# Kernel optimization log

Hardware: AMD Instinct MI355X
Metric: run time of the kernel (lower is better)

Reference implementation:

```python
import jax, jax.numpy as jnp
import numpy as np

CARRY_DIM = 384
READ_DIM = 128
D_MODEL = CARRY_DIM + READ_DIM  # 512
VOCAB = 128
NUM_FF = 7
B, T = 128, 1024


def _pm1(key, shape):
    # random +/-1 floats, matching random_pm1 in the torch source
    return jnp.where(jax.random.bernoulli(key, 0.5, shape), 1.0, -1.0).astype(jnp.float32)


def setup_inputs() -> dict:
    key = jax.random.key(0)
    k0, k1, k2, k3, k4 = jax.random.split(key, 5)
    return {
        "tokens": jax.random.randint(k0, (B, T), 0, VOCAB, dtype=jnp.int32),
        "initial": _pm1(k1, (D_MODEL,)),
        "embed": _pm1(k2, (VOCAB, READ_DIM)),
        "ff": _pm1(k3, (NUM_FF, D_MODEL, D_MODEL)),
        "ff_thresh": jnp.zeros((NUM_FF, D_MODEL), jnp.float32),
        "head": _pm1(k4, (READ_DIM, VOCAB)),
    }


def reference(tokens, initial, embed, ff, ff_thresh, head):
    # tokens:[B,T] int32; all params are +/-1 floats (the unpacked view of the
    # bit-packed int32 buffers; popcount GEMM == +/-1 matmul in integer arithmetic).
    b = tokens.shape[0]
    emb = jnp.swapaxes(embed[tokens], 0, 1)          # [T,B,READ_DIM]
    state0 = jnp.broadcast_to(initial, (b, D_MODEL))  # [B,512] +/-1

    def step(state, e):
        # replace read slice with current token embedding
        x = jnp.concatenate([state[:, :CARRY_DIM], e], axis=1)  # [B,512]

        def layer(xc, wt):
            w, t = wt  # w:[512,512], t:[512]
            # binary matmul (popcount dot in +/-1 space) + threshold nonlinearity
            return jnp.where(xc @ w >= t, 1.0, -1.0).astype(jnp.float32), None

        x, _ = jax.lax.scan(layer, x, (ff, ff_thresh))
        logits = x[:, CARRY_DIM:] @ head  # [B,VOCAB] integer-valued counts
        return x, logits

    _, logits = jax.lax.scan(step, state0, emb)  # logits:[T,B,V]
    return jnp.swapaxes(logits, 0, 1)            # [B,T,V]
```

## Files before the change

### kernel.cpp

```cpp
#include <hip/hip_runtime.h>
#include <hip/hip_bf16.h>
#include <stdint.h>
#include <math.h>

#define NUM_FF 7
#define DM 512
#define RD 128
#define VOCABN 128
#define BATCH 128
#define TLEN 1024

typedef unsigned int u32x4 __attribute__((ext_vector_type(4)));

__global__ void pack_ff_kernel(const float* __restrict__ ff, uint32_t* __restrict__ ffq) {
    int idx = blockIdx.x * blockDim.x + threadIdx.x;
    if (idx >= NUM_FF * 16 * DM) return;
    int j = idx & (DM - 1);
    int m = (idx >> 9) & 15;
    int l = idx >> 13;
    const float* base = ff + (size_t)l * DM * DM + (size_t)(m * 32) * DM + j;
    uint32_t w = 0;
#pragma unroll
    for (int i = 0; i < 32; ++i)
        w |= (base[(size_t)i * DM] > 0.0f ? 1u : 0u) << i;
    ffq[(l * 4 + (m >> 2)) * DM * 4 + j * 4 + (m & 3)] = w;
}

__global__ void pack_thresh_kernel(const float* __restrict__ th, int* __restrict__ it) {
    int idx = blockIdx.x * blockDim.x + threadIdx.x;
    if (idx < NUM_FF * DM)
        it[idx] = (int)floor((512.0 - (double)th[idx]) * 0.5);
}

__global__ void pack_small_kernel(const float* __restrict__ embed,
                                  const float* __restrict__ head,
                                  const float* __restrict__ initial,
                                  uint32_t* __restrict__ embp,
                                  uint32_t* __restrict__ headp,
                                  uint32_t* __restrict__ initp) {
    int idx = threadIdx.x;
    {
        int v = idx >> 2, k = idx & 3;
        uint32_t w = 0;
#pragma unroll
        for (int i = 0; i < 32; ++i)
            w |= (embed[v * RD + k * 32 + i] > 0.0f ? 1u : 0u) << i;
        embp[idx] = w;
    }
    {
        int k = idx >> 7, v = idx & 127;
        uint32_t w = 0;
#pragma unroll
        for (int i = 0; i < 32; ++i)
            w |= (head[(k * 32 + i) * VOCABN + v] > 0.0f ? 1u : 0u) << i;
        headp[idx] = w;
    }
    if (idx < 16) {
        uint32_t w = 0;
#pragma unroll
        for (int i = 0; i < 32; ++i)
            w |= (initial[idx * 32 + i] > 0.0f ? 1u : 0u) << i;
        initp[idx] = w;
    }
}

__device__ __forceinline__ int bdot4(uint4 s0, uint4 s1, uint4 s2, uint4 s3,
                                     u32x4 w0, u32x4 w1, u32x4 w2, u32x4 w3) {
    int a = __popc(s0.x ^ w0[0]);
    a += __popc(s0.y ^ w0[1]);
    a += __popc(s0.z ^ w0[2]);
    a += __popc(s0.w ^ w0[3]);
    a += __popc(s1.x ^ w1[0]);
    a += __popc(s1.y ^ w1[1]);
    a += __popc(s1.z ^ w1[2]);
    a += __popc(s1.w ^ w1[3]);
    int c = __popc(s2.x ^ w2[0]);
    c += __popc(s2.y ^ w2[1]);
    c += __popc(s2.z ^ w2[2]);
    c += __popc(s2.w ^ w2[3]);
    c += __popc(s3.x ^ w3[0]);
    c += __popc(s3.y ^ w3[1]);
    c += __popc(s3.z ^ w3[2]);
    c += __popc(s3.w ^ w3[3]);
    return a + c;
}

#define SYNCB asm volatile("s_waitcnt lgkmcnt(0)\n\ts_barrier" ::: "memory")

__attribute__((amdgpu_flat_work_group_size(512, 512), amdgpu_waves_per_eu(2, 2)))
__global__ void brnn_kernel(const int* __restrict__ tokens,
                            const uint32_t* __restrict__ ffq,
                            const int* __restrict__ ithr,
                            const uint32_t* __restrict__ embp,
                            const uint32_t* __restrict__ headp,
                            const uint32_t* __restrict__ initp,
                            float* __restrict__ out) {
    const int b = blockIdx.x;
    const int tid = threadIdx.x;
    const int wv = tid >> 6;
    const int lane = tid & 63;

    __shared__ uint4 xq0[4], xq1[4];
    __shared__ uint4 hx4;
    __shared__ uint32_t emb_lds[DM];
    __shared__ int tok_lds[TLEN + 2];

    u32x4 W00, W01, W02, W03, W10, W11, W12, W13, W20, W21, W22, W23,
          W30, W31, W32, W33, W40, W41, W42, W43, W50, W51, W52, W53,
          W60, W61, W62, W63;
#define WLOAD(V, L, Q) asm volatile("global_load_dwordx4 %0, %1, off" \
        : "=v"(V) : "v"(ffq + ((L) * 4 + (Q)) * (DM * 4) + tid * 4))
    WLOAD(W00, 0, 0); WLOAD(W01, 0, 1); WLOAD(W02, 0, 2); WLOAD(W03, 0, 3);
    WLOAD(W10, 1, 0); WLOAD(W11, 1, 1); WLOAD(W12, 1, 2); WLOAD(W13, 1, 3);
    WLOAD(W20, 2, 0); WLOAD(W21, 2, 1); WLOAD(W22, 2, 2); WLOAD(W23, 2, 3);
    WLOAD(W30, 3, 0); WLOAD(W31, 3, 1); WLOAD(W32, 3, 2); WLOAD(W33, 3, 3);
    WLOAD(W40, 4, 0); WLOAD(W41, 4, 1); WLOAD(W42, 4, 2); WLOAD(W43, 4, 3);
    WLOAD(W50, 5, 0); WLOAD(W51, 5, 1); WLOAD(W52, 5, 2); WLOAD(W53, 5, 3);
    WLOAD(W60, 6, 0); WLOAD(W61, 6, 1); WLOAD(W62, 6, 2); WLOAD(W63, 6, 3);
#undef WLOAD
    asm volatile("s_waitcnt vmcnt(0)" ::: "memory");

    const int it0 = ithr[0 * DM + tid];
    const int it1 = ithr[1 * DM + tid];
    const int it2 = ithr[2 * DM + tid];
    const int it3 = ithr[3 * DM + tid];
    const int it4 = ithr[4 * DM + tid];
    const int it5 = ithr[5 * DM + tid];
    const int it6 = ithr[6 * DM + tid];

    const int hvv = (wv << 4) | (lane & 15);
    const uint32_t h0 = headp[0 * VOCABN + hvv];
    const uint32_t h1 = headp[1 * VOCABN + hvv];
    const uint32_t h2 = headp[2 * VOCABN + hvv];
    const uint32_t h3 = headp[3 * VOCABN + hvv];

    emb_lds[tid] = embp[tid];
    tok_lds[tid] = tokens[b * TLEN + tid];
    tok_lds[tid + 512] = tokens[b * TLEN + tid + 512];
    if (tid == 0) { tok_lds[TLEN] = 0; tok_lds[TLEN + 1] = 0; }
    if (tid < 16) ((uint32_t*)xq0)[tid] = initp[tid];
    __syncthreads();
    if (tid < 4) ((uint32_t*)xq0)[12 + tid] = emb_lds[tok_lds[0] * 4 + tid];
    __syncthreads();

    float* outb = out + (size_t)b * TLEN * VOCABN;

#define LAYER(L, SRCQ, DSTQ) do {                                              \
        const uint4* xb_ = (const uint4*)(SRCQ);                               \
        uint4 s0 = xb_[0], s1 = xb_[1], s2 = xb_[2], s3 = xb_[3];              \
        int acc = bdot4(s0, s1, s2, s3, W##L##0, W##L##1, W##L##2, W##L##3);   \
        unsigned long long m = __ballot(acc <= it##L);                         \
        if (lane == 0)                                                         \
            ((uint2*)(DSTQ))[wv] = make_uint2((uint32_t)m, (uint32_t)(m >> 32)); \
        SYNCB;                                                                 \
    } while (0)

#define LAYERF(SRCQ, DSTQ) do {                                                \
        const uint4* xb_ = (const uint4*)(SRCQ);                               \
        uint4 s0 = xb_[0], s1 = xb_[1], s2 = xb_[2], s3 = xb_[3];              \
        int acc = bdot4(s0, s1, s2, s3, W60, W61, W62, W63);                   \
        unsigned long long m = __ballot(acc <= it6);                           \
        if (lane == 0) {                                                       \
            uint2 v_ = make_uint2((uint32_t)m, (uint32_t)(m >> 32));           \
            if (wv < 6) ((uint2*)(DSTQ))[wv] = v_;                             \
            else ((uint2*)&hx4)[wv - 6] = v_;                                  \
        }                                                                      \
        if (wv == 7 && lane < 4) ((uint32_t*)(DSTQ))[12 + lane] = embw;        \
        SYNCB;                                                                 \
    } while (0)

#define STEP(AQ, BQ, T) do {                                                   \
                      \
        uint32_t embw = 0;                                                     \
        if (wv == 7) embw = emb_lds[tok_lds[(T) + 1] * 4 + (lane & 3)];        \
        LAYER(0, AQ, BQ);                                                      \
        LAYER(1, BQ, AQ);                                                      \
        LAYER(2, AQ, BQ);                                                      \
        LAYER(3, BQ, AQ);                                                      \
        LAYER(4, AQ, BQ);                                                      \
        LAYER(5, BQ, AQ);                                                      \
        LAYERF(AQ, BQ);                                                        \
        uint4 hv_ = hx4;                                                       \
        if (lane < 16) {                                                       \
            int hc = __popc(hv_.x ^ h0) + __popc(hv_.y ^ h1) +                 \
                     __popc(hv_.z ^ h2) + __popc(hv_.w ^ h3);                  \
            outb[(T) * VOCABN + hvv] = (float)(RD - 2 * hc);                   \
        }                                                                      \
    } while (0)

    for (int t = 0; t < TLEN; t += 2) {
        STEP(xq0, xq1, t);
        STEP(xq1, xq0, t + 1);
    }
#undef LAYER
#undef LAYERF
#undef STEP
}

extern "C" void kernel_launch(void* const* d_in, const int* in_sizes, int n_in,
                              void* d_out, int out_size, void* d_ws, size_t ws_size,
                              hipStream_t stream) {
    const int* tokens = (const int*)d_in[0];
    const float* initial = (const float*)d_in[1];
    const float* embed = (const float*)d_in[2];
    const float* ff = (const float*)d_in[3];
    const float* ff_thresh = (const float*)d_in[4];
    const float* head = (const float*)d_in[5];
    float* out = (float*)d_out;

    uint32_t* ffq = (uint32_t*)d_ws;
    uint32_t* embp = ffq + NUM_FF * 16 * DM;
    uint32_t* headp = embp + 512;
    uint32_t* initp = headp + 512;
    int* ithr = (int*)(initp + 16);

    pack_ff_kernel<<<(NUM_FF * 16 * DM + 255) / 256, 256, 0, stream>>>(ff, ffq);
    pack_thresh_kernel<<<(NUM_FF * DM + 255) / 256, 256, 0, stream>>>(ff_thresh, ithr);
    pack_small_kernel<<<1, 512, 0, stream>>>(embed, head, initial, embp, headp, initp);
    brnn_kernel<<<BATCH, 512, 0, stream>>>(tokens, ffq, ithr, embp, headp, initp, out);
}
```

Baseline: 1.946 ms.

## Split each neuron's dot product across four lanes with DPP reduction and AGPR weights

```diff
diff --git a/kernel.cpp b/kernel.cpp
--- a/kernel.cpp
+++ b/kernel.cpp
@@ -13,17 +13,20 @@
 typedef unsigned int u32x4 __attribute__((ext_vector_type(4)));
 
 __global__ void pack_ff_kernel(const float* __restrict__ ff, uint32_t* __restrict__ ffq) {
-    int idx = blockIdx.x * blockDim.x + threadIdx.x;
-    if (idx >= NUM_FF * 16 * DM) return;
-    int j = idx & (DM - 1);
-    int m = (idx >> 9) & 15;
-    int l = idx >> 13;
-    const float* base = ff + (size_t)l * DM * DM + (size_t)(m * 32) * DM + j;
+    int o = blockIdx.x * blockDim.x + threadIdx.x;
+    if (o >= NUM_FF * 16 * DM) return;
+    int k = o & 3;
+    int t = (o >> 2) & (DM - 1);
+    int lq = o >> 11;
+    int l = lq >> 2, j = lq & 3;
+    int col = (t & ~3) + j;
+    int wi = 4 * (t & 3) + k;
+    const float* base = ff + (size_t)l * DM * DM + (size_t)(wi * 32) * DM + col;
     uint32_t w = 0;
 #pragma unroll
     for (int i = 0; i < 32; ++i)
         w |= (base[(size_t)i * DM] > 0.0f ? 1u : 0u) << i;
-    ffq[(l * 4 + (m >> 2)) * DM * 4 + j * 4 + (m & 3)] = w;
+    ffq[o] = w;
 }
 
 __global__ void pack_thresh_kernel(const float* __restrict__ th, int* __restrict__ it) {
@@ -39,16 +42,14 @@
                                   uint32_t* __restrict__ headp,
                                   uint32_t* __restrict__ initp) {
     int idx = threadIdx.x;
-    {
-        int v = idx >> 2, k = idx & 3;
+    {   int v = idx >> 2, k = idx & 3;
         uint32_t w = 0;
 #pragma unroll
         for (int i = 0; i < 32; ++i)
             w |= (embed[v * RD + k * 32 + i] > 0.0f ? 1u : 0u) << i;
         embp[idx] = w;
     }
-    {
-        int k = idx >> 7, v = idx & 127;
+    {   int k = idx >> 7, v = idx & 127;
         uint32_t w = 0;
 #pragma unroll
         for (int i = 0; i < 32; ++i)
@@ -64,28 +65,17 @@
     }
 }
 
-__device__ __forceinline__ int bdot4(uint4 s0, uint4 s1, uint4 s2, uint4 s3,
-                                     u32x4 w0, u32x4 w1, u32x4 w2, u32x4 w3) {
-    int a = __popc(s0.x ^ w0[0]);
-    a += __popc(s0.y ^ w0[1]);
-    a += __popc(s0.z ^ w0[2]);
-    a += __popc(s0.w ^ w0[3]);
-    a += __popc(s1.x ^ w1[0]);
-    a += __popc(s1.y ^ w1[1]);
-    a += __popc(s1.z ^ w1[2]);
-    a += __popc(s1.w ^ w1[3]);
-    int c = __popc(s2.x ^ w2[0]);
-    c += __popc(s2.y ^ w2[1]);
-    c += __popc(s2.z ^ w2[2]);
-    c += __popc(s2.w ^ w2[3]);
-    c += __popc(s3.x ^ w3[0]);
-    c += __popc(s3.y ^ w3[1]);
-    c += __popc(s3.z ^ w3[2]);
-    c += __popc(s3.w ^ w3[3]);
-    return a + c;
+__device__ __forceinline__ int dppadd(int v) {
+    v += __builtin_amdgcn_update_dpp(0, v, 0xB1, 0xF, 0xF, true);
+    v += __builtin_amdgcn_update_dpp(0, v, 0x4E, 0xF, 0xF, true);
+    return v;
 }
 
 #define SYNCB asm volatile("s_waitcnt lgkmcnt(0)\n\ts_barrier" ::: "memory")
+
+#define AW(D, S) asm volatile("v_accvgpr_write_b32 %0, %1" : "=a"(D) : "v"(S))
+#define AR(S) __extension__({ uint32_t r_; \
+        asm volatile("v_accvgpr_read_b32 %0, %1" : "=v"(r_) : "a"(S)); r_; })
 
 __attribute__((amdgpu_flat_work_group_size(512, 512), amdgpu_waves_per_eu(2, 2)))
 __global__ void brnn_kernel(const int* __restrict__ tokens,
@@ -99,21 +89,41 @@
     const int tid = threadIdx.x;
     const int wv = tid >> 6;
     const int lane = tid & 63;
+    const int lq4 = lane & 3;
 
     __shared__ uint4 xq0[4], xq1[4];
     __shared__ uint4 hx4;
     __shared__ uint32_t emb_lds[DM];
     __shared__ int tok_lds[TLEN + 2];
 
-    u32x4 W00, W01, W02, W03, W10, W11, W12, W13, W20, W21, W22, W23,
-          W30, W31, W32, W33, W40, W41, W42, W43, W50, W51, W52, W53,
-          W60, W61, W62, W63;
+    uint32_t A0_00,A0_01,A0_02,A0_03,A0_10,A0_11,A0_12,A0_13,
+             A0_20,A0_21,A0_22,A0_23,A0_30,A0_31,A0_32,A0_33;
+    uint32_t A1_00,A1_01,A1_02,A1_03,A1_10,A1_11,A1_12,A1_13,
+             A1_20,A1_21,A1_22,A1_23,A1_30,A1_31,A1_32,A1_33;
+    uint32_t A2_00,A2_01,A2_02,A2_03,A2_10,A2_11,A2_12,A2_13,
+             A2_20,A2_21,A2_22,A2_23,A2_30,A2_31,A2_32,A2_33;
+    uint32_t A3_00,A3_01,A3_02,A3_03,A3_10,A3_11,A3_12,A3_13,
+             A3_20,A3_21,A3_22,A3_23,A3_30,A3_31,A3_32,A3_33;
+
 #define WLOAD(V, L, Q) asm volatile("global_load_dwordx4 %0, %1, off" \
         : "=v"(V) : "v"(ffq + ((L) * 4 + (Q)) * (DM * 4) + tid * 4))
-    WLOAD(W00, 0, 0); WLOAD(W01, 0, 1); WLOAD(W02, 0, 2); WLOAD(W03, 0, 3);
-    WLOAD(W10, 1, 0); WLOAD(W11, 1, 1); WLOAD(W12, 1, 2); WLOAD(W13, 1, 3);
-    WLOAD(W20, 2, 0); WLOAD(W21, 2, 1); WLOAD(W22, 2, 2); WLOAD(W23, 2, 3);
-    WLOAD(W30, 3, 0); WLOAD(W31, 3, 1); WLOAD(W32, 3, 2); WLOAD(W33, 3, 3);
+
+#define AGLOAD(L) do { u32x4 t0_, t1_, t2_, t3_;                               \
+        WLOAD(t0_, L, 0); WLOAD(t1_, L, 1); WLOAD(t2_, L, 2); WLOAD(t3_, L, 3);\
+        asm volatile("s_waitcnt vmcnt(0)" ::: "memory");                       \
+        AW(A##L##_00, t0_[0]); AW(A##L##_01, t0_[1]);                          \
+        AW(A##L##_02, t0_[2]); AW(A##L##_03, t0_[3]);                          \
+        AW(A##L##_10, t1_[0]); AW(A##L##_11, t1_[1]);                          \
+        AW(A##L##_12, t1_[2]); AW(A##L##_13, t1_[3]);                          \
+        AW(A##L##_20, t2_[0]); AW(A##L##_21, t2_[1]);                          \
+        AW(A##L##_22, t2_[2]); AW(A##L##_23, t2_[3]);                          \
+        AW(A##L##_30, t3_[0]); AW(A##L##_31, t3_[1]);                          \
+        AW(A##L##_32, t3_[2]); AW(A##L##_33, t3_[3]);                          \
+    } while (0)
+
+    AGLOAD(0); AGLOAD(1); AGLOAD(2); AGLOAD(3);
+
+    u32x4 W40, W41, W42, W43, W50, W51, W52, W53, W60, W61, W62, W63;
     WLOAD(W40, 4, 0); WLOAD(W41, 4, 1); WLOAD(W42, 4, 2); WLOAD(W43, 4, 3);
     WLOAD(W50, 5, 0); WLOAD(W51, 5, 1); WLOAD(W52, 5, 2); WLOAD(W53, 5, 3);
     WLOAD(W60, 6, 0); WLOAD(W61, 6, 1); WLOAD(W62, 6, 2); WLOAD(W63, 6, 3);
@@ -145,20 +155,46 @@
 
     float* outb = out + (size_t)b * TLEN * VOCABN;
 
-#define LAYER(L, SRCQ, DSTQ) do {                                              \
-        const uint4* xb_ = (const uint4*)(SRCQ);                               \
-        uint4 s0 = xb_[0], s1 = xb_[1], s2 = xb_[2], s3 = xb_[3];              \
-        int acc = bdot4(s0, s1, s2, s3, W##L##0, W##L##1, W##L##2, W##L##3);   \
+#define QDOTV(a, xs, W) \
+        int a = __popc(xs.x ^ W[0]); a += __popc(xs.y ^ W[1]); \
+        a += __popc(xs.z ^ W[2]); a += __popc(xs.w ^ W[3])
+
+#define QLAYER_V(L, SRCQ, DSTQ) do {                                           \
+        uint4 xs = (SRCQ)[lq4];                                                \
+        QDOTV(a0, xs, W##L##0); QDOTV(a1, xs, W##L##1);                        \
+        QDOTV(a2, xs, W##L##2); QDOTV(a3, xs, W##L##3);                        \
+        a0 = dppadd(a0); a1 = dppadd(a1); a2 = dppadd(a2); a3 = dppadd(a3);    \
+        int acc = lq4 == 0 ? a0 : (lq4 == 1 ? a1 : (lq4 == 2 ? a2 : a3));      \
         unsigned long long m = __ballot(acc <= it##L);                         \
         if (lane == 0)                                                         \
             ((uint2*)(DSTQ))[wv] = make_uint2((uint32_t)m, (uint32_t)(m >> 32)); \
         SYNCB;                                                                 \
     } while (0)
 
-#define LAYERF(SRCQ, DSTQ) do {                                                \
-        const uint4* xb_ = (const uint4*)(SRCQ);                               \
-        uint4 s0 = xb_[0], s1 = xb_[1], s2 = xb_[2], s3 = xb_[3];              \
-        int acc = bdot4(s0, s1, s2, s3, W60, W61, W62, W63);                   \
+#define QDOTA(a, xs, L, J) \
+        int a = __popc(xs.x ^ AR(A##L##_##J##0)); \
+        a += __popc(xs.y ^ AR(A##L##_##J##1)); \
+        a += __popc(xs.z ^ AR(A##L##_##J##2)); \
+        a += __popc(xs.w ^ AR(A##L##_##J##3))
+
+#define QLAYER_A(L, SRCQ, DSTQ) do {                                           \
+        uint4 xs = (SRCQ)[lq4];                                                \
+        QDOTA(a0, xs, L, 0); QDOTA(a1, xs, L, 1);                              \
+        QDOTA(a2, xs, L, 2); QDOTA(a3, xs, L, 3);                              \
+        a0 = dppadd(a0); a1 = dppadd(a1); a2 = dppadd(a2); a3 = dppadd(a3);    \
+        int acc = lq4 == 0 ? a0 : (lq4 == 1 ? a1 : (lq4 == 2 ? a2 : a3));      \
+        unsigned long long m = __ballot(acc <= it##L);                         \
+        if (lane == 0)                                                         \
+            ((uint2*)(DSTQ))[wv] = make_uint2((uint32_t)m, (uint32_t)(m >> 32)); \
+        SYNCB;                                                                 \
+    } while (0)
+
+#define QLAYERF(SRCQ, DSTQ) do {                                               \
+        uint4 xs = (SRCQ)[lq4];                                                \
+        QDOTV(a0, xs, W60); QDOTV(a1, xs, W61);                                \
+        QDOTV(a2, xs, W62); QDOTV(a3, xs, W63);                                \
+        a0 = dppadd(a0); a1 = dppadd(a1); a2 = dppadd(a2); a3 = dppadd(a3);    \
+        int acc = lq4 == 0 ? a0 : (lq4 == 1 ? a1 : (lq4 == 2 ? a2 : a3));      \
         unsigned long long m = __ballot(acc <= it6);                           \
         if (lane == 0) {                                                       \
             uint2 v_ = make_uint2((uint32_t)m, (uint32_t)(m >> 32));           \
@@ -170,16 +206,15 @@
     } while (0)
 
 #define STEP(AQ, BQ, T) do {                                                   \
-                      \
         uint32_t embw = 0;                                                     \
         if (wv == 7) embw = emb_lds[tok_lds[(T) + 1] * 4 + (lane & 3)];        \
-        LAYER(0, AQ, BQ);                                                      \
-        LAYER(1, BQ, AQ);                                                      \
-        LAYER(2, AQ, BQ);                                                      \
-        LAYER(3, BQ, AQ);                                                      \
-        LAYER(4, AQ, BQ);                                                      \
-        LAYER(5, BQ, AQ);                                                      \
-        LAYERF(AQ, BQ);                                                        \
+        QLAYER_A(0, AQ, BQ);                                                   \
+        QLAYER_A(1, BQ, AQ);                                                   \
+        QLAYER_A(2, AQ, BQ);                                                   \
+        QLAYER_A(3, BQ, AQ);                                                   \
+        QLAYER_V(4, AQ, BQ);                                                   \
+        QLAYER_V(5, BQ, AQ);                                                   \
+        QLAYERF(AQ, BQ);                                                       \
         uint4 hv_ = hx4;                                                       \
         if (lane < 16) {                                                       \
             int hc = __popc(hv_.x ^ h0) + __popc(hv_.y ^ h1) +                 \
@@ -192,9 +227,6 @@
         STEP(xq0, xq1, t);
         STEP(xq1, xq0, t + 1);
     }
-#undef LAYER
-#undef LAYERF
-#undef STEP
 }
 
 extern "C" void kernel_launch(void* const* d_in, const int* in_sizes, int n_in,
```

After: 2.152 ms. 10.6% more time.
